# Kernel tuning notes

Measured on AMD Instinct MI355X. Metric: run time of the kernel, lower is better.

## Reference

```python
import jax, jax.numpy as jnp
import numpy as np

N, M, ND, K = 80000, 150000, 10000, 27  # active voxels, 2D painted points, downscaled voxels, 3x3x3 kernel
C3, C2, CP = 16, 64, 259                # 3D ch (stage 1), 2D conv ch, painted 2D feature ch
CM, CO = C3 + C2, 32 + 64               # mixed ch (80), downscale out ch (96)


def subm_conv(feats, nbr, W):
    """Submanifold sparse conv as gather + per-offset GEMM.
    feats: [N_in, Cin], nbr: [N_out, K] int (-1 = missing), W: [K, Cin, Cout]."""
    out = jnp.zeros((nbr.shape[0], W.shape[-1]), feats.dtype)
    for k in range(W.shape[0]):  # fixed small kernel loop (27)
        idx = nbr[:, k]
        g = jnp.where((idx >= 0)[:, None], feats[jnp.clip(idx, 0)], 0.0)
        out = out + g @ W[k]
    return out


def bn_relu(x, gamma, beta):  # folded eval-mode BN1d + ReLU
    return jax.nn.relu(x * gamma + beta)


def setup_inputs() -> dict:
    key = jax.random.key(0)
    ks = jax.random.split(key, 24)

    def w(k, shape, fan_in):
        return jax.random.normal(k, shape, jnp.float32) * (1.0 / np.sqrt(fan_in))

    inp = {
        'x3d': jax.random.normal(ks[0], (N, C3), jnp.float32),
        'f2d': jax.random.normal(ks[1], (M, CP), jnp.float32),
        'nn_idx': jax.random.randint(ks[2], (N,), -1, M, jnp.int32),     # -1 = no 2D match
        'nbr': jax.random.randint(ks[3], (N, K), -1, N, jnp.int32),      # -1 = missing neighbor
        'nbr_ds': jax.random.randint(ks[4], (ND, K), -1, N, jnp.int32),
        'W3d': w(ks[5], (K, C3, C3), K * C3),
        'g3d': jnp.ones((C3,), jnp.float32), 'b3d': jnp.zeros((C3,), jnp.float32),
        'Wg': w(ks[6], (C3, CP), C3), 'bg': jnp.zeros((CP,), jnp.float32),
        'Wc': w(ks[7], (C3, CP), C3), 'bc': jnp.zeros((CP,), jnp.float32),
        'Wp': w(ks[8], (CP, C2), CP),
        'W2d': w(ks[9], (K, C2, C2), K * C2),
        'g2d': jnp.ones((C2,), jnp.float32), 'b2d': jnp.zeros((C2,), jnp.float32),
        'Wm1': w(ks[10], (K, CM, CM), K * CM),
        'gm1': jnp.ones((CM,), jnp.float32), 'bm1': jnp.zeros((CM,), jnp.float32),
        'Wm2': w(ks[11], (K, CM, CM), K * CM),
        'gm2': jnp.ones((CM,), jnp.float32), 'bm2': jnp.zeros((CM,), jnp.float32),
        'Wa1': w(ks[12], (K, CM, CM), K * CM),
        'ga1': jnp.ones((CM,), jnp.float32), 'ba1': jnp.zeros((CM,), jnp.float32),
        'Wa2': w(ks[13], (K, CM, CM), K * CM),
        'ga2': jnp.ones((CM,), jnp.float32), 'ba2': jnp.zeros((CM,), jnp.float32),
        'Wds': w(ks[14], (K, CM, CO), K * CM),
        'gds': jnp.ones((CO,), jnp.float32), 'bds': jnp.zeros((CO,), jnp.float32),
    }
    return inp


def reference(x3d, f2d, nn_idx, nbr, nbr_ds,
              W3d, g3d, b3d, Wg, bg, Wc, bc, Wp,
              W2d, g2d, b2d,
              Wm1, gm1, bm1, Wm2, gm2, bm2,
              Wa1, ga1, ba1, Wa2, ga2, ba2,
              Wds, gds, bds):
    # irregular gather of painted 2D features to voxel sites (NN index, -1 invalid)
    f2g = jnp.where((nn_idx >= 0)[:, None], f2d[jnp.clip(nn_idx, 0)], 0.0)  # [N, 259]

    # 3D branch: SubMConv3d(C3->C3) + BN + ReLU
    y3d = bn_relu(subm_conv(x3d, nbr, W3d), g3d, b3d)                       # [N, 16]

    # per-stage gate / cross-gate (Linear + ReLU) on 3D features, applied to raw 2D feats
    gate = jax.nn.relu(y3d @ Wg + bg)                                       # [N, 259]
    cross = jax.nn.relu(y3d @ Wc + bc)                                      # [N, 259]

    # gated 2D branch: project gated painted feats to 64, SubMConv3d + BN + ReLU
    p2d = (gate * f2g) @ Wp                                                 # [N, 64]
    x2d = bn_relu(subm_conv(p2d, nbr, W2d), g2d, b2d)                       # [N, 64]
    cross2d = (cross * f2g) @ Wp                                            # [N, 64]

    # cross-modal mix + SparseBasicBlock (residual, two subm convs)
    mix = jnp.concatenate([y3d, x2d + cross2d], axis=-1)                    # [N, 80]
    h = bn_relu(subm_conv(mix, nbr, Wm1), gm1, bm1)
    h = jax.nn.relu(subm_conv(h, nbr, Wm2) * gm2 + bm2 + mix)

    # aggregation SparseBasicBlock
    a = bn_relu(subm_conv(h, nbr, Wa1), ga1, ba1)
    a = jax.nn.relu(subm_conv(a, nbr, Wa2) * ga2 + ba2 + h)

    # strided SparseConv3d downscale (gather from input sites at new out sites)
    out = bn_relu(subm_conv(a, nbr_ds, Wds), gds, bds)                      # [ND, 96]
    return out
```

## Files before the change

kernel.cpp:

```cpp
#include <hip/hip_runtime.h>

#define NPTS 80000
#define MPTS 150000
#define NDPTS 10000
#define KOFF 27
#define C3 16
#define CP 259
#define C2 64
#define CM 80
#define CO 96

typedef __attribute__((ext_vector_type(8))) short short8;
typedef __attribute__((ext_vector_type(4))) float f32x4;

__device__ inline short bf16r(float f) {
  union { float f; unsigned u; } x{f};
  unsigned r = (x.u + 0x7fffu + ((x.u >> 16) & 1u)) >> 16;
  return (short)r;
}

__global__ void wfrag_kernel(const float* __restrict__ W, short* __restrict__ WbfF,
                             int CIN, int COUT_, int KC) {
  const int NT = COUT_ / 16;
  int i = blockIdx.x * 256 + threadIdx.x;
  int total = KOFF * KC * NT * 512;
  if (i >= total) return;
  int j = i & 7, lane = (i >> 3) & 63;
  int rest = i >> 9;
  int t = rest % NT; rest /= NT;
  int q = rest % KC;
  int k = rest / KC;
  int ci = q * 32 + (lane >> 4) * 8 + j;
  int n = t * 16 + (lane & 15);
  float v = (ci < CIN) ? W[((size_t)k * CIN + ci) * COUT_ + n] : 0.f;
  WbfF[i] = bf16r(v);
}

__global__ void wpfrag_kernel(const float* __restrict__ Wp, short* __restrict__ WpF) {
  int i = blockIdx.x * 256 + threadIdx.x;
  if (i >= 9 * 4 * 64 * 8) return;
  int j = i & 7, lane = (i >> 3) & 63, t = (i >> 9) & 3, q = i >> 11;
  int k = q * 32 + (lane >> 4) * 8 + j;
  int n = t * 16 + (lane & 15);
  WpF[i] = (k < CP) ? bf16r(Wp[(size_t)k * C2 + n]) : (short)0;
}

__global__ __launch_bounds__(256) void conv3d_bnrelu_kernel(
    const float* __restrict__ x3d, const int* __restrict__ nbr,
    const float* __restrict__ W3d, const float* __restrict__ g3d,
    const float* __restrict__ b3d, float* __restrict__ y3d,
    float* __restrict__ mix, short* __restrict__ mixbf)
{
  __shared__ float wS[KOFF * C3 * C3];
  __shared__ float fS[16][C3];
  const int tid = threadIdx.x;
  const int base = blockIdx.x * 16;
  for (int e = tid; e < KOFF * C3 * C3; e += 256) wS[e] = W3d[e];
  const int r = tid >> 4, c = tid & 15;
  const int row = base + r;
  float acc = 0.f;
  for (int k = 0; k < KOFF; ++k) {
    int idx = nbr[row * KOFF + k];
    float fv = (idx >= 0) ? x3d[idx * C3 + c] : 0.f;
    __syncthreads();
    fS[r][c] = fv;
    __syncthreads();
    const float* wk = &wS[k * C3 * C3];
    #pragma unroll
    for (int ci = 0; ci < C3; ++ci)
      acc = fmaf(fS[r][ci], wk[ci * C3 + c], acc);
  }
  float v = fmaxf(fmaf(acc, g3d[c], b3d[c]), 0.f);
  y3d[row * C3 + c] = v;
  mix[row * CM + c] = v;
  mixbf[row * CM + c] = bf16r(v);
}

__global__ __launch_bounds__(256) void gate_cross_mfma_kernel(
    const float* __restrict__ y3d, const float* __restrict__ f2d,
    const int* __restrict__ nn_idx,
    const float* __restrict__ Wg, const float* __restrict__ bg,
    const float* __restrict__ Wc, const float* __restrict__ bc,
    const short* __restrict__ WpF,
    short* __restrict__ p2dbf, float* __restrict__ cross2d)
{
  constexpr int RS = 296;
  __shared__ short g1S[32 * RS];
  __shared__ short g2S[32 * RS];
  const int tid = threadIdx.x;
  const int lane = tid & 63;
  const int w = tid >> 6;
  const int lm = lane & 15;
  const int quad = lane >> 4;
  const int base = blockIdx.x * 32;

  for (int e = tid; e < 32 * 32; e += 256) {
    int r = e >> 5, cc = 256 + (e & 31);
    if (cc >= CP) {
      g1S[r * RS + cc] = 0;
      g2S[r * RS + cc] = 0;
    }
  }

  {
    const int c = tid;
    float wg[16], wc[16];
    #pragma unroll
    for (int ci = 0; ci < 16; ++ci) {
      wg[ci] = Wg[ci * CP + c];
      wc[ci] = Wc[ci * CP + c];
    }
    const float bgv = bg[c], bcv = bc[c];
    for (int r = 0; r < 32; ++r) {
      const int row = base + r;
      const int idx = nn_idx[row];
      const float* yr = y3d + (size_t)row * C3;
      float f = (idx >= 0) ? f2d[(size_t)idx * CP + c] : 0.f;
      float a1 = bgv, a2 = bcv;
      #pragma unroll
      for (int ci = 0; ci < 16; ++ci) {
        float yv = yr[ci];
        a1 = fmaf(yv, wg[ci], a1);
        a2 = fmaf(yv, wc[ci], a2);
      }
      g1S[r * RS + c] = bf16r(fmaxf(a1, 0.f) * f);
      g2S[r * RS + c] = bf16r(fmaxf(a2, 0.f) * f);
    }
  }
  if (w == 0 && lane < 3) {
    const int c = 256 + lane;
    float wg[16], wc[16];
    #pragma unroll
    for (int ci = 0; ci < 16; ++ci) {
      wg[ci] = Wg[ci * CP + c];
      wc[ci] = Wc[ci * CP + c];
    }
    const float bgv = bg[c], bcv = bc[c];
    for (int r = 0; r < 32; ++r) {
      const int row = base + r;
      const int idx = nn_idx[row];
      const float* yr = y3d + (size_t)row * C3;
      float f = (idx >= 0) ? f2d[(size_t)idx * CP + c] : 0.f;
      float a1 = bgv, a2 = bcv;
      #pragma unroll
      for (int ci = 0; ci < 16; ++ci) {
        float yv = yr[ci];
        a1 = fmaf(yv, wg[ci], a1);
        a2 = fmaf(yv, wc[ci], a2);
      }
      g1S[r * RS + c] = bf16r(fmaxf(a1, 0.f) * f);
      g2S[r * RS + c] = bf16r(fmaxf(a2, 0.f) * f);
    }
  }
  __syncthreads();

  const int gsel = w & 1;
  const int mt = w >> 1;
  const short* gS = gsel ? g2S : g1S;
  f32x4 acc[4];
  #pragma unroll
  for (int t = 0; t < 4; ++t) {
    f32x4 z = {0.f, 0.f, 0.f, 0.f};
    acc[t] = z;
  }
  #pragma unroll
  for (int q = 0; q < 9; ++q) {
    short8 af = *(const short8*)&gS[(mt * 16 + lm) * RS + q * 32 + quad * 8];
    #pragma unroll
    for (int t = 0; t < 4; ++t) {
      short8 bf = *(const short8*)&WpF[(((q * 4 + t) * 64) + lane) * 8];
      acc[t] = __builtin_amdgcn_mfma_f32_16x16x32_bf16(af, bf, acc[t], 0, 0, 0);
    }
  }
  #pragma unroll
  for (int t = 0; t < 4; ++t) {
    const int c = t * 16 + lm;
    #pragma unroll
    for (int rg = 0; rg < 4; ++rg) {
      const int row = base + mt * 16 + quad * 4 + rg;
      float v = acc[t][rg];
      if (gsel == 0)
        p2dbf[(size_t)row * C2 + c] = bf16r(v);
      else
        cross2d[(size_t)row * C2 + c] = v;
    }
  }
}

template <int CIN, int COUT_, int MODE, int MINW>
__global__ __launch_bounds__(256, MINW) void conv_db_kernel(
    const short* __restrict__ finbf, const int* __restrict__ nbr, int nrows,
    const short* __restrict__ WbfF, const float* __restrict__ gamma,
    const float* __restrict__ beta, const float* __restrict__ resf,
    float* __restrict__ outf, short* __restrict__ outbf)
{
  constexpr int KC = (CIN + 31) / 32;
  constexpr int KC32 = KC * 32;
  constexpr int AS = KC32 + 8;
  constexpr int PCH = KC32 / 8;
  constexpr int DCH = CIN / 8;
  constexpr int NT = COUT_ / 16;
  constexpr int MT = 2;
  constexpr int ROWS = 128;
  constexpr int AR = ROWS * PCH / 256;

  __shared__ short fA[2][ROWS * AS];

  const int tid = threadIdx.x;
  const int lane = tid & 63;
  const int w = tid >> 6;
  const int lm = lane & 15;
  const int quad = lane >> 4;
  const int base = blockIdx.x * ROWS;

  int ar[AR], ac[AR];
  #pragma unroll
  for (int i = 0; i < AR; ++i) {
    int j = tid + i * 256;
    ar[i] = j / PCH;
    ac[i] = j - ar[i] * PCH;
  }

  f32x4 acc[MT][NT];
  #pragma unroll
  for (int i = 0; i < MT; ++i)
    #pragma unroll
    for (int t = 0; t < NT; ++t) {
      f32x4 z = {0.f, 0.f, 0.f, 0.f};
      acc[i][t] = z;
    }

  const short8 zero8 = {0, 0, 0, 0, 0, 0, 0, 0};
  short8 pa[AR];

  #pragma unroll
  for (int i = 0; i < AR; ++i) {
    int row = base + ar[i];
    int ix = (row < nrows) ? nbr[(size_t)row * KOFF] : -1;
    pa[i] = (ix >= 0 && ac[i] < DCH)
        ? *(const short8*)&finbf[(size_t)ix * CIN + ac[i] * 8] : zero8;
  }
  #pragma unroll
  for (int i = 0; i < AR; ++i)
    *(short8*)&fA[0][ar[i] * AS + ac[i] * 8] = pa[i];
  __syncthreads();

  for (int k = 0; k < KOFF; ++k) {
    const int cur = k & 1;
    if (k + 1 < KOFF) {
      #pragma unroll
      for (int i = 0; i < AR; ++i) {
        int row = base + ar[i];
        int ix = (row < nrows) ? nbr[(size_t)row * KOFF + k + 1] : -1;
        pa[i] = (ix >= 0 && ac[i] < DCH)
            ? *(const short8*)&finbf[(size_t)ix * CIN + ac[i] * 8] : zero8;
      }
    }
    #pragma unroll
    for (int q = 0; q < KC; ++q) {
      short8 afr[MT];
      #pragma unroll
      for (int i = 0; i < MT; ++i)
        afr[i] = *(const short8*)&fA[cur][((w * MT + i) * 16 + lm) * AS +
                                          q * 32 + quad * 8];
      #pragma unroll
      for (int t = 0; t < NT; ++t) {
        short8 bfr = *(const short8*)&WbfF[(size_t)(((k * KC + q) * NT + t) * 512) +
                                           lane * 8];
        #pragma unroll
        for (int i = 0; i < MT; ++i)
          acc[i][t] = __builtin_amdgcn_mfma_f32_16x16x32_bf16(afr[i], bfr,
                                                              acc[i][t], 0, 0, 0);
      }
    }
    if (k + 1 < KOFF) {
      #pragma unroll
      for (int i = 0; i < AR; ++i)
        *(short8*)&fA[cur ^ 1][ar[i] * AS + ac[i] * 8] = pa[i];
    }
    __syncthreads();
  }

  #pragma unroll
  for (int i = 0; i < MT; ++i) {
    int rbase = base + (w * MT + i) * 16 + quad * 4;
    #pragma unroll
    for (int t = 0; t < NT; ++t) {
      int c = t * 16 + lm;
      float g = gamma[c], b = beta[c];
      #pragma unroll
      for (int rg = 0; rg < 4; ++rg) {
        int row = rbase + rg;
        if (row >= nrows) continue;
        float v = acc[i][t][rg];
        if (MODE == 0) {
          outf[(size_t)row * COUT_ + c] = fmaxf(fmaf(v, g, b), 0.f);
        } else if (MODE == 1) {
          outbf[(size_t)row * COUT_ + c] = bf16r(fmaxf(fmaf(v, g, b), 0.f));
        } else if (MODE == 2) {
          float o = fmaxf(fmaf(v, g, b), 0.f) + resf[(size_t)row * C2 + c];
          outf[(size_t)row * CM + 16 + c] = o;
          outbf[(size_t)row * CM + 16 + c] = bf16r(o);
        } else if (MODE == 3) {
          float o = fmaxf(fmaf(v, g, b) + resf[(size_t)row * COUT_ + c], 0.f);
          outf[(size_t)row * COUT_ + c] = o;
          outbf[(size_t)row * COUT_ + c] = bf16r(o);
        } else {
          float o = fmaxf(fmaf(v, g, b) + resf[(size_t)row * COUT_ + c], 0.f);
          outbf[(size_t)row * COUT_ + c] = bf16r(o);
        }
      }
    }
  }
}

extern "C" void kernel_launch(void* const* d_in, const int* in_sizes, int n_in,
                              void* d_out, int out_size, void* d_ws, size_t ws_size,
                              hipStream_t stream) {
  const float* x3d  = (const float*)d_in[0];
  const float* f2d  = (const float*)d_in[1];
  const int*   nn   = (const int*)d_in[2];
  const int*   nbr  = (const int*)d_in[3];
  const int*   nbds = (const int*)d_in[4];
  const float* W3d  = (const float*)d_in[5];
  const float* g3d  = (const float*)d_in[6];
  const float* b3d  = (const float*)d_in[7];
  const float* Wg   = (const float*)d_in[8];
  const float* bg   = (const float*)d_in[9];
  const float* Wc   = (const float*)d_in[10];
  const float* bc   = (const float*)d_in[11];
  const float* Wp   = (const float*)d_in[12];
  const float* W2d  = (const float*)d_in[13];
  const float* g2d  = (const float*)d_in[14];
  const float* b2d  = (const float*)d_in[15];
  const float* Wm1  = (const float*)d_in[16];
  const float* gm1  = (const float*)d_in[17];
  const float* bm1  = (const float*)d_in[18];
  const float* Wm2  = (const float*)d_in[19];
  const float* gm2  = (const float*)d_in[20];
  const float* bm2  = (const float*)d_in[21];
  const float* Wa1  = (const float*)d_in[22];
  const float* ga1  = (const float*)d_in[23];
  const float* ba1  = (const float*)d_in[24];
  const float* Wa2  = (const float*)d_in[25];
  const float* ga2  = (const float*)d_in[26];
  const float* ba2  = (const float*)d_in[27];
  const float* Wds  = (const float*)d_in[28];
  const float* gds  = (const float*)d_in[29];
  const float* bds  = (const float*)d_in[30];

  const size_t N = NPTS;
  float* ws = (float*)d_ws;
  float* y3d     = ws;
  short* p2dbf   = (short*)(ws + N * 16);
  float* cross2d = ws + N * 48;
  float* mix     = ws + N * 112;
  short* mixbf   = (short*)(ws + N * 192);
  short* tmp1bf  = (short*)(ws + N * 232);
  float* hbuf    = ws + N * 272;
  short* hbufbf  = (short*)(ws + N * 352);
  short* abufbf  = (short*)ws;
  short* wtail  = (short*)(ws + N * 392);
  short* WbfF2d = wtail;
  short* WbfFm1 = WbfF2d + 110592;
  short* WbfFm2 = WbfFm1 + 207360;
  short* WbfFa1 = WbfFm2 + 207360;
  short* WbfFa2 = WbfFa1 + 207360;
  short* WbfFds = WbfFa2 + 207360;
  short* WpF    = WbfFds + 248832;

  wfrag_kernel<<<(110592 + 255) / 256, 256, 0, stream>>>(W2d, WbfF2d, 64, 64, 2);
  wfrag_kernel<<<(207360 + 255) / 256, 256, 0, stream>>>(Wm1, WbfFm1, 80, 80, 3);
  wfrag_kernel<<<(207360 + 255) / 256, 256, 0, stream>>>(Wm2, WbfFm2, 80, 80, 3);
  wfrag_kernel<<<(207360 + 255) / 256, 256, 0, stream>>>(Wa1, WbfFa1, 80, 80, 3);
  wfrag_kernel<<<(207360 + 255) / 256, 256, 0, stream>>>(Wa2, WbfFa2, 80, 80, 3);
  wfrag_kernel<<<(248832 + 255) / 256, 256, 0, stream>>>(Wds, WbfFds, 80, 96, 3);
  wpfrag_kernel<<<(9 * 4 * 64 * 8 + 255) / 256, 256, 0, stream>>>(Wp, WpF);

  conv3d_bnrelu_kernel<<<NPTS / 16, 256, 0, stream>>>(x3d, nbr, W3d, g3d, b3d,
                                                      y3d, mix, mixbf);
  gate_cross_mfma_kernel<<<NPTS / 32, 256, 0, stream>>>(y3d, f2d, nn, Wg, bg,
                                                        Wc, bc, WpF, p2dbf,
                                                        cross2d);

  const int gridN = (NPTS + 127) / 128;
  conv_db_kernel<64, 64, 2, 4><<<gridN, 256, 0, stream>>>(
      p2dbf, nbr, NPTS, WbfF2d, g2d, b2d, cross2d, mix, mixbf);
  conv_db_kernel<80, 80, 1, 3><<<gridN, 256, 0, stream>>>(
      mixbf, nbr, NPTS, WbfFm1, gm1, bm1, nullptr, nullptr, tmp1bf);
  conv_db_kernel<80, 80, 3, 3><<<gridN, 256, 0, stream>>>(
      tmp1bf, nbr, NPTS, WbfFm2, gm2, bm2, mix, hbuf, hbufbf);
  conv_db_kernel<80, 80, 1, 3><<<gridN, 256, 0, stream>>>(
      hbufbf, nbr, NPTS, WbfFa1, ga1, ba1, nullptr, nullptr, tmp1bf);
  conv_db_kernel<80, 80, 4, 3><<<gridN, 256, 0, stream>>>(
      tmp1bf, nbr, NPTS, WbfFa2, ga2, ba2, hbuf, nullptr, abufbf);

  const int gridND = (NDPTS + 127) / 128;
  conv_db_kernel<80, 96, 0, 3><<<gridND, 256, 0, stream>>>(
      abufbf, nbds, NDPTS, WbfFds, gds, bds, nullptr, (float*)d_out, nullptr);
}
```

Before: 1.144 ms.

## Move stage-1 3D conv to bf16 MFMA and deepen gather prefetch in convs

Replaces the scalar fp32 16-channel submanifold conv with an MFMA kernel. It packs two kernel offsets per 32-wide K chunk, using pre-fragmented bf16 weights and a bf16 copy of x3d, with double-buffered LDS gathers. The gate/cross kernel now prefetches the next row's f2d value, and the generic conv kernel loads neighbor indices two offsets ahead so the gather latency overlaps the MFMA work. The stage-1 conv gains bf16 rounding error, and the extra prefetch buffers raise register pressure.

```diff
diff --git a/kernel.cpp b/kernel.cpp
--- a/kernel.cpp
+++ b/kernel.cpp
@@ -11,6 +11,7 @@
 #define CO 96
 
 typedef __attribute__((ext_vector_type(8))) short short8;
+typedef __attribute__((ext_vector_type(4))) short s16x4;
 typedef __attribute__((ext_vector_type(4))) float f32x4;
 
 __device__ inline short bf16r(float f) {
@@ -45,35 +46,98 @@
   WpF[i] = (k < CP) ? bf16r(Wp[(size_t)k * C2 + n]) : (short)0;
 }
 
-__global__ __launch_bounds__(256) void conv3d_bnrelu_kernel(
-    const float* __restrict__ x3d, const int* __restrict__ nbr,
-    const float* __restrict__ W3d, const float* __restrict__ g3d,
+__global__ void w3dfrag_kernel(const float* __restrict__ W3d, short* __restrict__ W3dF) {
+  int i = blockIdx.x * 256 + threadIdx.x;
+  if (i >= 14 * 512) return;
+  int j = i & 7, lane = (i >> 3) & 63, q = i >> 9;
+  int kci = q * 32 + (lane >> 4) * 8 + j;
+  int o = kci >> 4, ci = kci & 15, n = lane & 15;
+  W3dF[i] = (o < KOFF) ? bf16r(W3d[((size_t)o * C3 + ci) * C3 + n]) : (short)0;
+}
+
+__global__ void x3dprep_kernel(const float* __restrict__ x3d, short* __restrict__ x3dbf) {
+  int i = blockIdx.x * 256 + threadIdx.x;
+  if (i < NPTS * C3) x3dbf[i] = bf16r(x3d[i]);
+}
+
+__global__ __launch_bounds__(256, 4) void conv3d_mfma_kernel(
+    const short* __restrict__ x3dbf, const int* __restrict__ nbr,
+    const short* __restrict__ W3dF, const float* __restrict__ g3d,
     const float* __restrict__ b3d, float* __restrict__ y3d,
     float* __restrict__ mix, short* __restrict__ mixbf)
 {
-  __shared__ float wS[KOFF * C3 * C3];
-  __shared__ float fS[16][C3];
+  constexpr int QCH = 14;
+  constexpr int AS3 = 40;
+  __shared__ short fA[2][128 * AS3];
   const int tid = threadIdx.x;
-  const int base = blockIdx.x * 16;
-  for (int e = tid; e < KOFF * C3 * C3; e += 256) wS[e] = W3d[e];
-  const int r = tid >> 4, c = tid & 15;
-  const int row = base + r;
-  float acc = 0.f;
-  for (int k = 0; k < KOFF; ++k) {
-    int idx = nbr[row * KOFF + k];
-    float fv = (idx >= 0) ? x3d[idx * C3 + c] : 0.f;
-    __syncthreads();
-    fS[r][c] = fv;
-    __syncthreads();
-    const float* wk = &wS[k * C3 * C3];
-    #pragma unroll
-    for (int ci = 0; ci < C3; ++ci)
-      acc = fmaf(fS[r][ci], wk[ci * C3 + c], acc);
-  }
-  float v = fmaxf(fmaf(acc, g3d[c], b3d[c]), 0.f);
-  y3d[row * C3 + c] = v;
-  mix[row * CM + c] = v;
-  mixbf[row * CM + c] = bf16r(v);
+  const int lane = tid & 63;
+  const int w = tid >> 6;
+  const int lm = lane & 15;
+  const int quad = lane >> 4;
+  const int base = blockIdx.x * 128;
+
+  int srow[4], sc[4];
+  #pragma unroll
+  for (int i = 0; i < 4; ++i) {
+    int j = tid + i * 256;
+    srow[i] = j >> 3;
+    sc[i] = j & 7;
+  }
+
+  f32x4 acc[2];
+  #pragma unroll
+  for (int i = 0; i < 2; ++i) { f32x4 z = {0.f,0.f,0.f,0.f}; acc[i] = z; }
+
+  const s16x4 zero4 = {0, 0, 0, 0};
+  s16x4 pa[4];
+
+#define GATH3(Q)                                                            \
+  _Pragma("unroll") for (int i = 0; i < 4; ++i) {                           \
+    int o = 2 * (Q) + (sc[i] >> 2);                                         \
+    int ix = (o < KOFF) ? nbr[(size_t)(base + srow[i]) * KOFF + o] : -1;    \
+    pa[i] = (ix >= 0)                                                       \
+        ? *(const s16x4*)&x3dbf[(size_t)ix * C3 + (sc[i] & 3) * 4] : zero4; \
+  }
+#define WR3(B)                                                              \
+  _Pragma("unroll") for (int i = 0; i < 4; ++i)                             \
+    *(s16x4*)&fA[B][srow[i] * AS3 + (sc[i] >> 2) * 16 + (sc[i] & 3) * 4] = pa[i];
+
+  GATH3(0)
+  WR3(0)
+  __syncthreads();
+
+  for (int q = 0; q < QCH; ++q) {
+    if (q + 1 < QCH) { GATH3(q + 1) }
+    short8 af[2];
+    #pragma unroll
+    for (int i = 0; i < 2; ++i)
+      af[i] = *(const short8*)&fA[q & 1][((w * 2 + i) * 16 + lm) * AS3 + quad * 8];
+    short8 bfr = *(const short8*)&W3dF[(size_t)q * 512 + lane * 8];
+    #pragma unroll
+    for (int i = 0; i < 2; ++i)
+      acc[i] = __builtin_amdgcn_mfma_f32_16x16x32_bf16(af[i], bfr, acc[i], 0, 0, 0);
+    if (q + 1 < QCH) {
+      WR3((q + 1) & 1)
+      __syncthreads();
+    }
+  }
+#undef GATH3
+#undef WR3
+
+  const int c = lm;
+  const float g = g3d[c], b = b3d[c];
+  #pragma unroll
+  for (int i = 0; i < 2; ++i) {
+    int rbase = base + (w * 2 + i) * 16 + quad * 4;
+    #pragma unroll
+    for (int rg = 0; rg < 4; ++rg) {
+      int row = rbase + rg;
+      float v = fmaxf(fmaf(acc[i][rg], g, b), 0.f);
+      y3d[(size_t)row * C3 + c] = v;
+      mix[(size_t)row * CM + c] = v;
+      mixbf[(size_t)row * CM + c] = bf16r(v);
+    }
+  }
 }
 
 __global__ __launch_bounds__(256) void gate_cross_mfma_kernel(
@@ -111,11 +175,15 @@
       wc[ci] = Wc[ci * CP + c];
     }
     const float bgv = bg[c], bcv = bc[c];
+    int idx0 = nn_idx[base];
+    float fnext = (idx0 >= 0) ? f2d[(size_t)idx0 * CP + c] : 0.f;
     for (int r = 0; r < 32; ++r) {
-      const int row = base + r;
-      const int idx = nn_idx[row];
-      const float* yr = y3d + (size_t)row * C3;
-      float f = (idx >= 0) ? f2d[(size_t)idx * CP + c] : 0.f;
+      float f = fnext;
+      if (r + 1 < 32) {
+        int idxn = nn_idx[base + r + 1];
+        fnext = (idxn >= 0) ? f2d[(size_t)idxn * CP + c] : 0.f;
+      }
+      const float* yr = y3d + (size_t)(base + r) * C3;
       float a1 = bgv, a2 = bcv;
       #pragma unroll
       for (int ci = 0; ci < 16; ++ci) {
@@ -159,10 +227,7 @@
   const short* gS = gsel ? g2S : g1S;
   f32x4 acc[4];
   #pragma unroll
-  for (int t = 0; t < 4; ++t) {
-    f32x4 z = {0.f, 0.f, 0.f, 0.f};
-    acc[t] = z;
-  }
+  for (int t = 0; t < 4; ++t) { f32x4 z = {0.f,0.f,0.f,0.f}; acc[t] = z; }
   #pragma unroll
   for (int q = 0; q < 9; ++q) {
     short8 af = *(const short8*)&gS[(mt * 16 + lm) * RS + q * 32 + quad * 8];
@@ -213,73 +278,95 @@
   const int quad = lane >> 4;
   const int base = blockIdx.x * ROWS;
 
-  int ar[AR], ac[AR];
+  int ar[AR], ac[AR], rw[AR];
+  bool av[AR], rv[AR];
   #pragma unroll
   for (int i = 0; i < AR; ++i) {
     int j = tid + i * 256;
     ar[i] = j / PCH;
     ac[i] = j - ar[i] * PCH;
+    av[i] = ac[i] < DCH;
+    rw[i] = base + ar[i];
+    rv[i] = rw[i] < nrows;
   }
 
   f32x4 acc[MT][NT];
   #pragma unroll
   for (int i = 0; i < MT; ++i)
     #pragma unroll
-    for (int t = 0; t < NT; ++t) {
-      f32x4 z = {0.f, 0.f, 0.f, 0.f};
-      acc[i][t] = z;
-    }
+    for (int t = 0; t < NT; ++t) { f32x4 z = {0.f,0.f,0.f,0.f}; acc[i][t] = z; }
 
   const short8 zero8 = {0, 0, 0, 0, 0, 0, 0, 0};
-  short8 pa[AR];
-
-  #pragma unroll
-  for (int i = 0; i < AR; ++i) {
-    int row = base + ar[i];
-    int ix = (row < nrows) ? nbr[(size_t)row * KOFF] : -1;
-    pa[i] = (ix >= 0 && ac[i] < DCH)
-        ? *(const short8*)&finbf[(size_t)ix * CIN + ac[i] * 8] : zero8;
-  }
-  #pragma unroll
-  for (int i = 0; i < AR; ++i)
-    *(short8*)&fA[0][ar[i] * AS + ac[i] * 8] = pa[i];
-  __syncthreads();
-
-  for (int k = 0; k < KOFF; ++k) {
-    const int cur = k & 1;
-    if (k + 1 < KOFF) {
-      #pragma unroll
-      for (int i = 0; i < AR; ++i) {
-        int row = base + ar[i];
-        int ix = (row < nrows) ? nbr[(size_t)row * KOFF + k + 1] : -1;
-        pa[i] = (ix >= 0 && ac[i] < DCH)
-            ? *(const short8*)&finbf[(size_t)ix * CIN + ac[i] * 8] : zero8;
-      }
-    }
-    #pragma unroll
-    for (int q = 0; q < KC; ++q) {
-      short8 afr[MT];
-      #pragma unroll
-      for (int i = 0; i < MT; ++i)
-        afr[i] = *(const short8*)&fA[cur][((w * MT + i) * 16 + lm) * AS +
-                                          q * 32 + quad * 8];
-      #pragma unroll
-      for (int t = 0; t < NT; ++t) {
-        short8 bfr = *(const short8*)&WbfF[(size_t)(((k * KC + q) * NT + t) * 512) +
-                                           lane * 8];
-        #pragma unroll
-        for (int i = 0; i < MT; ++i)
-          acc[i][t] = __builtin_amdgcn_mfma_f32_16x16x32_bf16(afr[i], bfr,
-                                                              acc[i][t], 0, 0, 0);
-      }
-    }
-    if (k + 1 < KOFF) {
-      #pragma unroll
-      for (int i = 0; i < AR; ++i)
-        *(short8*)&fA[cur ^ 1][ar[i] * AS + ac[i] * 8] = pa[i];
-    }
+  short8 pa[2][AR];
+  int pidx[2][AR];
+
+  {
+    int ix0[AR];
+    #pragma unroll
+    for (int i = 0; i < AR; ++i)
+      ix0[i] = rv[i] ? nbr[(size_t)rw[i] * KOFF + 0] : -1;
+    #pragma unroll
+    for (int i = 0; i < AR; ++i)
+      pidx[1][i] = rv[i] ? nbr[(size_t)rw[i] * KOFF + 1] : -1;
+    #pragma unroll
+    for (int i = 0; i < AR; ++i)
+      pidx[0][i] = rv[i] ? nbr[(size_t)rw[i] * KOFF + 2] : -1;
+    short8 t0[AR];
+    #pragma unroll
+    for (int i = 0; i < AR; ++i)
+      t0[i] = (ix0[i] >= 0 && av[i])
+          ? *(const short8*)&finbf[(size_t)ix0[i] * CIN + ac[i] * 8] : zero8;
+    #pragma unroll
+    for (int i = 0; i < AR; ++i) {
+      int ix = pidx[1][i];
+      pa[1][i] = (ix >= 0 && av[i])
+          ? *(const short8*)&finbf[(size_t)ix * CIN + ac[i] * 8] : zero8;
+    }
+    #pragma unroll
+    for (int i = 0; i < AR; ++i)
+      *(short8*)&fA[0][ar[i] * AS + ac[i] * 8] = t0[i];
     __syncthreads();
   }
+
+#define KITER(K, S)                                                             \
+  {                                                                             \
+    if ((K) + 3 < KOFF) {                                                       \
+      _Pragma("unroll") for (int i = 0; i < AR; ++i)                            \
+        pidx[S ^ 1][i] = rv[i] ? nbr[(size_t)rw[i] * KOFF + (K) + 3] : -1;      \
+    }                                                                           \
+    if ((K) + 2 < KOFF) {                                                       \
+      _Pragma("unroll") for (int i = 0; i < AR; ++i) {                          \
+        int ix = pidx[S][i];                                                    \
+        pa[S][i] = (ix >= 0 && av[i])                                           \
+            ? *(const short8*)&finbf[(size_t)ix * CIN + ac[i] * 8] : zero8;     \
+      }                                                                         \
+    }                                                                           \
+    _Pragma("unroll") for (int q = 0; q < KC; ++q) {                            \
+      short8 afr[MT];                                                           \
+      _Pragma("unroll") for (int i = 0; i < MT; ++i)                            \
+        afr[i] = *(const short8*)&fA[S][((w * MT + i) * 16 + lm) * AS +         \
+                                        q * 32 + quad * 8];                     \
+      _Pragma("unroll") for (int t = 0; t < NT; ++t) {                          \
+        short8 bfr = *(const short8*)&WbfF[(size_t)((((K) * KC + q) * NT + t) * \
+                                                    512) + lane * 8];           \
+        _Pragma("unroll") for (int i = 0; i < MT; ++i)                          \
+          acc[i][t] = __builtin_amdgcn_mfma_f32_16x16x32_bf16(afr[i], bfr,      \
+                                                              acc[i][t], 0, 0, 0); \
+      }                                                                         \
+    }                                                                           \
+    if ((K) + 1 < KOFF) {                                                       \
+      _Pragma("unroll") for (int i = 0; i < AR; ++i)                            \
+        *(short8*)&fA[S ^ 1][ar[i] * AS + ac[i] * 8] = pa[S ^ 1][i];            \
+      __syncthreads();                                                          \
+    }                                                                           \
+  }
+
+  for (int kk = 0; kk + 2 < KOFF; kk += 2) {
+    KITER(kk, 0)
+    KITER(kk + 1, 1)
+  }
+  KITER(KOFF - 1, 0)
+#undef KITER
 
   #pragma unroll
   for (int i = 0; i < MT; ++i) {
@@ -354,6 +441,7 @@
   float* y3d     = ws;
   short* p2dbf   = (short*)(ws + N * 16);
   float* cross2d = ws + N * 48;
+  short* x3dbf   = (short*)(ws + N * 48);
   float* mix     = ws + N * 112;
   short* mixbf   = (short*)(ws + N * 192);
   short* tmp1bf  = (short*)(ws + N * 232);
@@ -368,6 +456,7 @@
   short* WbfFa2 = WbfFa1 + 207360;
   short* WbfFds = WbfFa2 + 207360;
   short* WpF    = WbfFds + 248832;
+  short* W3dF   = WpF + 18432;
 
   wfrag_kernel<<<(110592 + 255) / 256, 256, 0, stream>>>(W2d, WbfF2d, 64, 64, 2);
   wfrag_kernel<<<(207360 + 255) / 256, 256, 0, stream>>>(Wm1, WbfFm1, 80, 80, 3);
@@ -376,9 +465,11 @@
   wfrag_kernel<<<(207360 + 255) / 256, 256, 0, stream>>>(Wa2, WbfFa2, 80, 80, 3);
   wfrag_kernel<<<(248832 + 255) / 256, 256, 0, stream>>>(Wds, WbfFds, 80, 96, 3);
   wpfrag_kernel<<<(9 * 4 * 64 * 8 + 255) / 256, 256, 0, stream>>>(Wp, WpF);
-
-  conv3d_bnrelu_kernel<<<NPTS / 16, 256, 0, stream>>>(x3d, nbr, W3d, g3d, b3d,
-                                                      y3d, mix, mixbf);
+  w3dfrag_kernel<<<(14 * 512 + 255) / 256, 256, 0, stream>>>(W3d, W3dF);
+  x3dprep_kernel<<<(NPTS * C3 + 255) / 256, 256, 0, stream>>>(x3d, x3dbf);
+
+  conv3d_mfma_kernel<<<NPTS / 128, 256, 0, stream>>>(x3dbf, nbr, W3dF, g3d, b3d,
+                                                     y3d, mix, mixbf);
   gate_cross_mfma_kernel<<<NPTS / 32, 256, 0, stream>>>(y3d, f2d, nn, Wg, bg,
                                                         Wc, bc, WpF, p2dbf,
                                                         cross2d);
```

After: 1.219 ms. +6.5%, slower.
